# Kernel tuning notes

Hardware: AMD Instinct MI355X
Metric: run time of the kernel (lower is better)

Reference implementation:

```python
import jax, jax.numpy as jnp
import numpy as np

B, M, D, H, W = 8, 36, 512, 14, 14
T = 64
HW = H * W
N = M * HW
GAMMA1, GAMMA2, GAMMA3 = 4.0, 5.0, 10.0


def setup_inputs() -> dict:
    key = jax.random.key(0)
    k1, k2 = jax.random.split(key)
    image = jax.random.normal(k1, (B, M, D, H, W), dtype=jnp.float32) * 0.1
    text = jax.random.normal(k2, (B, T, D), dtype=jnp.float32) * 0.1
    length_info = jnp.full((B,), T, dtype=jnp.int32)
    rng = np.random.RandomState(0)
    sp = rng.randint(0, B, size=(B, 5)).astype(np.int32)
    sp[:, 0] = np.arange(B)  # spinds[0] = i in the original loop
    spinds = jnp.asarray(sp)
    return {"image": image, "text": text, "length_info": length_info, "spinds": spinds}


def matching_score(v, e):
    """v: (N, D) flattened region features, e: (T, D) word features.
    Returns (scalar score R_QD + R_QD2, beta (T, M))."""
    sim = e @ v.T                                   # (T, N)
    norm_sim = jax.nn.softmax(sim, axis=0)          # softmax over words
    attn = jax.nn.softmax(GAMMA1 * norm_sim, axis=1)  # softmax over regions
    v_tidal = attn @ v                              # (T, D)
    diag = jnp.sum(v_tidal * e, axis=1)             # diag(v_tidal @ e.T), (T,)
    r_qd = (1.0 / GAMMA2) * jnp.log(jnp.sum(jnp.exp(diag * GAMMA2)))

    sim_exp = jnp.exp(norm_sim).reshape(T, M, HW)
    local_sum = jnp.sum(sim_exp, axis=(0, 2))       # (M,) per-box total
    beta = jnp.sum(sim_exp, axis=2) / local_sum     # (T, M)

    e_prime = e.T @ beta                            # (D, M)
    v_r = v.reshape(M, HW, D)
    ve = jnp.einsum('mnd,dm->mn', v_r, e_prime)     # (M, HW)
    row_norm = jnp.linalg.norm(v_r, axis=2)         # (M, HW)
    ep_norm = jnp.linalg.norm(e_prime, axis=0)      # (M,)
    ref = jnp.sum(ve / (row_norm * ep_norm[:, None]), axis=1) / HW  # (M,)
    r_qd2 = (1.0 / GAMMA2) * jnp.log(jnp.sum(jnp.exp(ref)))
    return r_qd + r_qd2, beta


def _forward(image, text, spinds):
    # permute(0,3,2,1) then view(M*H_r*H_w, D): (M, D, H, W) -> (M, W, H, D)
    v_all = jnp.transpose(image, (0, 1, 4, 3, 2)).reshape(B, N, D)

    # pairwise matching score S[i, j] = score(v_i, e_j)
    S = jax.vmap(lambda vi: jax.vmap(lambda ej: matching_score(vi, ej)[0])(text))(v_all)  # (B, B)
    betas = jax.vmap(lambda vi, ei: matching_score(vi, ei)[1])(v_all, text)               # (B, T, M)

    numer = GAMMA3 * jnp.exp(jnp.diagonal(S))                       # (B,)
    # P_DQ_denum_i = sum_k gamma3 * exp(S[i, spinds[i,k]])
    p_dq = jnp.sum(GAMMA3 * jnp.exp(jnp.take_along_axis(S, spinds, axis=1)), axis=1)
    # P_QD_denum_i = sum_k gamma3 * exp(S[spinds[i,k], i])
    p_qd = jnp.sum(GAMMA3 * jnp.exp(jnp.take_along_axis(S.T, spinds, axis=1)), axis=1)

    loss1 = -jnp.mean(numer / p_dq)
    loss2 = -jnp.mean(numer / p_qd)

    tmp = jnp.einsum('btm,bsm->bts', betas, betas)                  # (B, T, T)
    diag2 = jnp.sum(jnp.diagonal(tmp, axis1=1, axis2=2) ** 2, axis=1)
    reg = jnp.sum(jnp.sqrt(jnp.sum(tmp ** 2, axis=(1, 2)) - diag2))
    loss_reg = reg / (B * T * M)
    return loss1 + loss2 + loss_reg


def reference(image, text, length_info, spinds):
    # length_info is full (== T) for every sample, so each e = text[i][:T].
    return _forward(image, text, spinds)
```

## Files before the change

kernel.cpp:

```cpp
#include <hip/hip_runtime.h>
#include <hip/hip_bf16.h>
#include <cstdint>

#define BB 8
#define MM 36
#define DD 512
#define TT 64
#define HWW 196
#define HWP 224
#define NN 7056
#define NNP 8064
#define NCK 252
#define NPAIR 64
#define G2c 5.0f
#define G3c 10.0f

typedef __attribute__((ext_vector_type(8))) short s8v;
typedef __attribute__((ext_vector_type(4))) float f4v;

__device__ __forceinline__ float bflySum(float v) {
#pragma unroll
  for (int off = 32; off > 0; off >>= 1) v += __shfl_xor(v, off, 64);
  return v;
}
__device__ __forceinline__ float bflyMax(float v) {
#pragma unroll
  for (int off = 32; off > 0; off >>= 1) v = fmaxf(v, __shfl_xor(v, off, 64));
  return v;
}
__device__ __forceinline__ unsigned short f2bf(float x) {
  __hip_bfloat16 h = __float2bfloat16(x);
  return *(unsigned short*)&h;
}
__device__ __forceinline__ float bf2f(unsigned short u) {
  unsigned int x = ((unsigned int)u) << 16;
  return __uint_as_float(x);
}

__global__ void p_text(const float* __restrict__ text,
                       unsigned short* __restrict__ eb) {
  int idx = blockIdx.x * 256 + threadIdx.x;
  eb[idx] = f2bf(text[idx]);
}

__global__ void __launch_bounds__(256) p_img(const float* __restrict__ image,
                                             unsigned int* __restrict__ imgbp) {
  int bm = blockIdx.x, ds = blockIdx.y;
  int tid = threadIdx.x;
  const float* src = image + ((size_t)bm * DD + ds * 32) * HWW;
  unsigned int* dst = imgbp + ((size_t)bm * DD + ds * 32) * (HWP / 2);
#pragma unroll
  for (int u = 0; u < 14; ++u) {
    int idx = tid + u * 256;
    int dl = idx / 112, hp = idx - dl * 112;
    int hw = hp * 2;
    unsigned int lo = 0, hi = 0;
    if (hp < 98) {
      lo = f2bf(src[(size_t)dl * HWW + hw]);
      hi = f2bf(src[(size_t)dl * HWW + hw + 1]);
    }
    dst[(size_t)dl * (HWP / 2) + hp] = lo | (hi << 16);
  }
}

__global__ void p_imgT(const float* __restrict__ image,
                       unsigned short* __restrict__ imgbp2) {
  __shared__ float tile[32][33];
  int bm = blockIdx.x;
  int hw0 = blockIdx.y * 32;
  int d0 = blockIdx.z * 32;
  int tx = threadIdx.x, ty = threadIdx.y;
  const float* src = image + ((size_t)bm * DD + d0) * HWW + hw0;
#pragma unroll
  for (int r = 0; r < 32; r += 8) {
    int d = r + ty;
    tile[d][tx] = (hw0 + tx < HWW) ? src[(size_t)d * HWW + tx] : 0.f;
  }
  __syncthreads();
  unsigned short* dst = imgbp2 + ((size_t)bm * HWP + hw0) * DD + d0;
#pragma unroll
  for (int r = 0; r < 32; r += 8) {
    int hwo = r + ty;
    dst[(size_t)hwo * DD + tx] = f2bf(tile[tx][hwo]);
  }
}

__global__ void __launch_bounds__(256) k1_mfma(
    const unsigned short* __restrict__ eb,
    const unsigned short* __restrict__ imgbp2,
    unsigned short* __restrict__ attnR,
    float* __restrict__ wpartg, float* __restrict__ apartg) {
  int ck = blockIdx.x;
  int i = blockIdx.y;
  int mi = ck / 7;
  int hwb = (ck - mi * 7) * 32;
  int bm = i * MM + mi;
  int tid = threadIdx.x;
  int w = tid >> 6, l = tid & 63;
  int g = l >> 4, c = l & 15;

  __shared__ unsigned short vsb[32][520];
  __shared__ unsigned short trb[512 * 32];

  const unsigned short* vsrc = imgbp2 + ((size_t)bm * HWP + hwb) * DD;
#pragma unroll
  for (int k = 0; k < 8; ++k) {
    int flat = tid * 8 + k * 2048;
    int row = flat >> 9, col = flat & 511;
    *(s8v*)&vsb[row][col] = *(const s8v*)(vsrc + (size_t)row * DD + col);
  }
  __syncthreads();

  f4v acc[8][2];
#pragma unroll
  for (int q = 0; q < 8; ++q)
#pragma unroll
    for (int nt = 0; nt < 2; ++nt) acc[q][nt] = (f4v){0.f, 0.f, 0.f, 0.f};

  for (int ks = 0; ks < 16; ++ks) {
    int d0 = ks * 32;
    s8v Bf0 = *(const s8v*)&vsb[c][d0 + g * 8];
    s8v Bf1 = *(const s8v*)&vsb[16 + c][d0 + g * 8];
#pragma unroll
    for (int q = 0; q < 8; ++q) {
      s8v Af = *(const s8v*)(eb + ((size_t)((w * 8 + q) * 16 + c)) * DD + d0 +
                             g * 8);
      acc[q][0] = __builtin_amdgcn_mfma_f32_16x16x32_bf16(Af, Bf0, acc[q][0], 0, 0, 0);
      acc[q][1] = __builtin_amdgcn_mfma_f32_16x16x32_bf16(Af, Bf1, acc[q][1], 0, 0, 0);
    }
  }

  float rz[2][2];
#pragma unroll
  for (int jj = 0; jj < 2; ++jj)
#pragma unroll
    for (int nt = 0; nt < 2; ++nt) {
      float mx = -3e38f;
#pragma unroll
      for (int qq = 0; qq < 4; ++qq)
#pragma unroll
        for (int r = 0; r < 4; ++r) mx = fmaxf(mx, acc[jj * 4 + qq][nt][r]);
      mx = fmaxf(mx, __shfl_xor(mx, 16, 64));
      mx = fmaxf(mx, __shfl_xor(mx, 32, 64));
      float z = 0.f;
#pragma unroll
      for (int qq = 0; qq < 4; ++qq)
#pragma unroll
        for (int r = 0; r < 4; ++r) {
          float p = expf(acc[jj * 4 + qq][nt][r] - mx);
          acc[jj * 4 + qq][nt][r] = p;
          z += p;
        }
      z += __shfl_xor(z, 16, 64);
      z += __shfl_xor(z, 32, 64);
      rz[jj][nt] = 1.f / z;
    }

#pragma unroll
  for (int q = 0; q < 8; ++q) {
    int jj = q >> 2;
#pragma unroll
    for (int r = 0; r < 4; ++r) {
      float wp = 0.f, ap = 0.f;
#pragma unroll
      for (int nt = 0; nt < 2; ++nt) {
        float ns = acc[q][nt][r] * rz[jj][nt];
        float w1 = expf(ns);
        float a2 = w1 * w1;
        float a4 = a2 * a2;
        bool valid = (hwb + nt * 16 + c) < HWW;
        float a4m = valid ? a4 : 0.f;
        trb[((w * 8 + q) * 16 + g * 4 + r) * 32 + nt * 16 + c] = f2bf(a4m);
        wp += valid ? w1 : 0.f;
        ap += a4m;
      }
#pragma unroll
      for (int off = 1; off < 16; off <<= 1) {
        wp += __shfl_xor(wp, off, 64);
        ap += __shfl_xor(ap, off, 64);
      }
      if (c == 0) {
        int t = (q & 3) * 16 + g * 4 + r;
        size_t pidx = ((size_t)(i * 8 + 2 * w + jj) * NCK + ck) * 64 + t;
        wpartg[pidx] = wp;
        apartg[pidx] = ap;
      }
    }
  }
  __syncthreads();
#pragma unroll
  for (int j = 0; j < 8; ++j) {
    unsigned short* dst =
        attnR + ((size_t)(i * 8 + j) * NCK + ck) * 2048 + tid * 8;
    *(s8v*)dst = *(const s8v*)&trb[j * 2048 + tid * 8];
  }
}

__global__ void __launch_bounds__(256) k_red(const float* __restrict__ wpartg,
                                             const float* __restrict__ apartg,
                                             float* __restrict__ sbuf,
                                             float* __restrict__ Abuf) {
  int pair = blockIdx.x;
  int tid = threadIdx.x;
  int t = tid & 63, part = tid >> 6;
  float s = 0.f;
  for (int ck = part; ck < NCK; ck += 4)
    s += apartg[((size_t)pair * NCK + ck) * 64 + t];
  __shared__ float ab[4][64];
  ab[part][t] = s;
  __syncthreads();
  if (tid < 64)
    Abuf[pair * 64 + tid] = ab[0][tid] + ab[1][tid] + ab[2][tid] + ab[3][tid];
  for (int idx = tid; idx < 64 * MM; idx += 256) {
    int tt = idx / MM, m = idx - (idx / MM) * MM;
    float ss = 0.f;
#pragma unroll
    for (int cc = 0; cc < 7; ++cc)
      ss += wpartg[((size_t)pair * NCK + m * 7 + cc) * 64 + tt];
    sbuf[((size_t)pair * TT + tt) * MM + m] = ss;
  }
}

__global__ void __launch_bounds__(256) k2_mfma(
    const unsigned short* __restrict__ attnR,
    const unsigned short* __restrict__ imgbp, float* __restrict__ vt_part) {
  int dh = blockIdx.x;
  int kslab = blockIdx.y;
  int pair = blockIdx.z;
  int i = pair >> 3;
  int tid = threadIdx.x;
  int w = tid >> 6, l = tid & 63;
  int g = l >> 4, c = l & 15;
  int d0b = dh * 256;

  __shared__ unsigned short asb[TT][40];
  __shared__ unsigned short bsb[256][40];

  f4v acc[4][4];
#pragma unroll
  for (int tt = 0; tt < 4; ++tt)
#pragma unroll
    for (int dd = 0; dd < 4; ++dd) acc[tt][dd] = (f4v){0.f, 0.f, 0.f, 0.f};

  for (int ks = 0; ks < 126; ++ks) {
    int ckg = kslab * 126 + ks;
    int n0 = ckg * 32;
    int mi = n0 / HWP, hw0 = n0 - mi * HWP;
    const unsigned short* bbase =
        imgbp + ((size_t)(i * MM + mi) * DD + d0b) * HWP + hw0;
    __syncthreads();
    {
      const unsigned short* ach = attnR + ((size_t)pair * NCK + ckg) * 2048;
      int t = tid >> 2, qq = tid & 3;
      *(s8v*)&asb[t][qq * 8] = *(const s8v*)(ach + tid * 8);
    }
#pragma unroll
    for (int u = 0; u < 4; ++u) {
      int idx = tid + u * 256;
      int d = idx >> 2, qq = idx & 3;
      *(s8v*)&bsb[d][qq * 8] = *(const s8v*)(bbase + (size_t)d * HWP + qq * 8);
    }
    __syncthreads();
    s8v Af[4];
#pragma unroll
    for (int tt = 0; tt < 4; ++tt)
      Af[tt] = *(const s8v*)&asb[tt * 16 + c][g * 8];
#pragma unroll
    for (int dd = 0; dd < 4; ++dd) {
      s8v Bf = *(const s8v*)&bsb[(w * 4 + dd) * 16 + c][g * 8];
#pragma unroll
      for (int tt = 0; tt < 4; ++tt)
        acc[tt][dd] = __builtin_amdgcn_mfma_f32_16x16x32_bf16(Af[tt], Bf,
                                                              acc[tt][dd], 0, 0, 0);
    }
  }
  float* op = vt_part + ((size_t)kslab * NPAIR + pair) * TT * DD;
#pragma unroll
  for (int tt = 0; tt < 4; ++tt)
#pragma unroll
    for (int dd = 0; dd < 4; ++dd)
#pragma unroll
      for (int r = 0; r < 4; ++r) {
        int t = tt * 16 + g * 4 + r;
        int d = d0b + (w * 4 + dd) * 16 + c;
        op[(size_t)t * DD + d] = acc[tt][dd][r];
      }
}

__global__ void __launch_bounds__(256) k2b_reduce(
    const float* __restrict__ vt_part, const float* __restrict__ Abuf,
    float* __restrict__ v_tidal) {
  size_t f = (size_t)blockIdx.x * 256 + threadIdx.x;
  size_t base = f * 4;
  const size_t slab = (size_t)NPAIR * TT * DD;
  float rA = 1.f / Abuf[base >> 9];
  float4 s0 = *(const float4*)&vt_part[base];
  float4 s1 = *(const float4*)&vt_part[slab + base];
  float4 r;
  r.x = (s0.x + s1.x) * rA;
  r.y = (s0.y + s1.y) * rA;
  r.z = (s0.z + s1.z) * rA;
  r.w = (s0.w + s1.w) * rA;
  *(float4*)&v_tidal[base] = r;
}

__global__ void __launch_bounds__(256) k3_rqd(
    const float* __restrict__ v_tidal, const float* __restrict__ text,
    float* __restrict__ r_qd) {
  int pair = blockIdx.x;
  int j = pair & 7;
  int lane = threadIdx.x & 63, wid = threadIdx.x >> 6;
  __shared__ float dg[TT];
  for (int tt = 0; tt < 16; ++tt) {
    int t = wid * 16 + tt;
    const float* vt = v_tidal + ((size_t)pair * TT + t) * DD;
    const float* e = text + ((size_t)j * TT + t) * DD;
    float a = 0.f;
#pragma unroll
    for (int k = 0; k < 8; ++k) {
      int d = k * 64 + lane;
      a = fmaf(vt[d], e[d], a);
    }
    a = bflySum(a);
    if (lane == 0) dg[t] = a;
  }
  __syncthreads();
  if (threadIdx.x < TT) {
    float v = dg[threadIdx.x] * G2c;
    float mxv = bflyMax(v);
    float zz = bflySum(expf(v - mxv));
    if (threadIdx.x == 0) r_qd[pair] = (mxv + logf(zz)) / G2c;
  }
}

__global__ void __launch_bounds__(256) k4_beta(const float* __restrict__ sbuf,
                                               float* __restrict__ beta) {
  int pair = blockIdx.x;
  __shared__ float sl[TT * MM];
  __shared__ float ls[MM];
  for (int idx = threadIdx.x; idx < TT * MM; idx += 256)
    sl[idx] = sbuf[(size_t)pair * TT * MM + idx];
  __syncthreads();
  if (threadIdx.x < MM) {
    float a = 0.f;
    for (int t = 0; t < TT; ++t) a += sl[t * MM + threadIdx.x];
    ls[threadIdx.x] = 1.f / a;
  }
  __syncthreads();
  for (int idx = threadIdx.x; idx < TT * MM; idx += 256) {
    int mcol = idx % MM;
    beta[(size_t)pair * TT * MM + idx] = sl[idx] * ls[mcol];
  }
}

__global__ void __launch_bounds__(256) k5_eprime(
    const float* __restrict__ text, const float* __restrict__ beta,
    float* __restrict__ e_prime, float* __restrict__ ep_norm) {
  int m = blockIdx.x, pair = blockIdx.y;
  int j = pair & 7;
  int d = threadIdx.x * 2;
  float a0 = 0.f, a1 = 0.f;
  const float* bt = beta + (size_t)pair * TT * MM + m;
  const float* e = text + (size_t)j * TT * DD + d;
  for (int t = 0; t < TT; ++t) {
    float b = bt[t * MM];
    float2 ev = *(const float2*)(e + (size_t)t * DD);
    a0 = fmaf(ev.x, b, a0);
    a1 = fmaf(ev.y, b, a1);
  }
  *(float2*)(e_prime + ((size_t)pair * MM + m) * DD + d) = make_float2(a0, a1);
  __shared__ float buf[4];
  float nr = bflySum(a0 * a0 + a1 * a1);
  int lane = threadIdx.x & 63, wid = threadIdx.x >> 6;
  if (lane == 0) buf[wid] = nr;
  __syncthreads();
  if (threadIdx.x == 0)
    ep_norm[pair * MM + m] = sqrtf(buf[0] + buf[1] + buf[2] + buf[3]);
}

__global__ void __launch_bounds__(256) k6_ref(
    const unsigned short* __restrict__ imgbp2,
    const float* __restrict__ e_prime, const float* __restrict__ ep_norm,
    float* __restrict__ refb) {
  int m = blockIdx.x, pair = blockIdx.y;
  int i = pair >> 3;
  int bm = i * MM + m;
  int tid = threadIdx.x, w = tid >> 6, l = tid & 63;
  const float* ep = e_prime + ((size_t)pair * MM + m) * DD + l * 8;
  float4 e0 = *(const float4*)ep;
  float4 e1 = *(const float4*)(ep + 4);
  float epr[8] = {e0.x, e0.y, e0.z, e0.w, e1.x, e1.y, e1.z, e1.w};
  float ren = 1.f / ep_norm[pair * MM + m];
  float accv = 0.f;
  for (int k = 0; k < 49; ++k) {
    int hw = w + 4 * k;
    s8v v8 = *(const s8v*)(imgbp2 + ((size_t)bm * HWP + hw) * DD + l * 8);
    float ve = 0.f, rn = 0.f;
#pragma unroll
    for (int e = 0; e < 8; ++e) {
      float vv = bf2f((unsigned short)v8[e]);
      ve = fmaf(vv, epr[e], ve);
      rn = fmaf(vv, vv, rn);
    }
    ve = bflySum(ve);
    rn = bflySum(rn);
    accv += ve * rsqrtf(rn) * ren;
  }
  __shared__ float buf[4];
  if (l == 0) buf[w] = accv;
  __syncthreads();
  if (tid == 0)
    refb[pair * MM + m] = (buf[0] + buf[1] + buf[2] + buf[3]) * (1.0f / HWW);
}

__global__ void k7_S(const float* __restrict__ refb,
                     const float* __restrict__ r_qd, float* __restrict__ Sb) {
  int pair = threadIdx.x;
  if (pair >= NPAIR) return;
  const float* r = refb + pair * MM;
  float mx = -1e30f;
  for (int mi = 0; mi < MM; ++mi) mx = fmaxf(mx, r[mi]);
  float z = 0.f;
  for (int mi = 0; mi < MM; ++mi) z += expf(r[mi] - mx);
  Sb[pair] = r_qd[pair] + (mx + logf(z)) / G2c;
}

__global__ void __launch_bounds__(256) k8a(const float* __restrict__ beta,
                                           float* __restrict__ sregs) {
  int b = blockIdx.x;
  __shared__ float bb[TT * MM];
  __shared__ float buf[4];
  int tid = threadIdx.x;
  size_t base = (size_t)(b * BB + b) * TT * MM;
  for (int idx = tid; idx < TT * MM; idx += 256) bb[idx] = beta[base + idx];
  __syncthreads();
  float val = 0.f;
  for (int k = 0; k < 16; ++k) {
    int idx = tid + k * 256;
    int t = idx >> 6, s2 = idx & 63;
    if (t != s2) {
      float dot = 0.f;
      for (int mi = 0; mi < MM; ++mi)
        dot = fmaf(bb[t * MM + mi], bb[s2 * MM + mi], dot);
      val += dot * dot;
    }
  }
  val = bflySum(val);
  int lane = tid & 63, wid = tid >> 6;
  if (lane == 0) buf[wid] = val;
  __syncthreads();
  if (tid == 0) sregs[b] = sqrtf(fmaxf(buf[0] + buf[1] + buf[2] + buf[3], 0.f));
}

__global__ void k8b(const float* __restrict__ Sb,
                    const float* __restrict__ sregs,
                    const int* __restrict__ spinds, float* __restrict__ out) {
  if (threadIdx.x != 0) return;
  float sreg = 0.f;
  for (int b = 0; b < BB; ++b) sreg += sregs[b];
  float l1 = 0.f, l2 = 0.f;
  for (int i = 0; i < BB; ++i) {
    float num = G3c * expf(Sb[i * BB + i]);
    float pdq = 0.f, pqd = 0.f;
    for (int k = 0; k < 5; ++k) {
      int kk = spinds[i * 5 + k];
      pdq += G3c * expf(Sb[i * BB + kk]);
      pqd += G3c * expf(Sb[kk * BB + i]);
    }
    l1 += num / pdq;
    l2 += num / pqd;
  }
  out[0] = -(l1 / BB) - (l2 / BB) + sreg / (float)(BB * TT * MM);
}

extern "C" void kernel_launch(void* const* d_in, const int* in_sizes, int n_in,
                              void* d_out, int out_size, void* d_ws,
                              size_t ws_size, hipStream_t stream) {
  const float* image = (const float*)d_in[0];
  const float* text = (const float*)d_in[1];
  const int* spinds = (const int*)d_in[3];
  float* out = (float*)d_out;

  float* ws = (float*)d_ws;
  size_t off = 0;
  unsigned short* attnR = (unsigned short*)(ws + off);
  off += (size_t)NPAIR * NCK * 2048 / 2;
  unsigned short* imgbp = (unsigned short*)(ws + off);
  off += (size_t)BB * MM * DD * HWP / 2;
  unsigned short* imgbp2 = (unsigned short*)(ws + off);
  off += (size_t)BB * MM * HWP * DD / 2;
  float* vt_part = ws + off; off += (size_t)2 * NPAIR * TT * DD;
  unsigned short* eb = (unsigned short*)(ws + off);
  off += (size_t)BB * TT * DD / 2;
  float* wpartg = ws + off;  off += (size_t)NPAIR * NCK * 64;
  float* apartg = ws + off;  off += (size_t)NPAIR * NCK * 64;
  float* Abuf = ws + off;    off += (size_t)NPAIR * TT;
  float* v_tidal = ws + off; off += (size_t)NPAIR * TT * DD;
  float* sbuf = ws + off;    off += (size_t)NPAIR * TT * MM;
  float* beta = ws + off;    off += (size_t)NPAIR * TT * MM;
  float* e_prime = ws + off; off += (size_t)NPAIR * MM * DD;
  float* ep_norm = ws + off; off += (size_t)NPAIR * MM;
  float* refb = ws + off;    off += (size_t)NPAIR * MM;
  float* r_qd = ws + off;    off += (size_t)NPAIR;
  float* Sb = ws + off;      off += (size_t)NPAIR;
  float* sregs = ws + off;   off += (size_t)BB;

  p_text<<<1024, 256, 0, stream>>>(text, eb);
  p_img<<<dim3(BB * MM, 16), 256, 0, stream>>>(image, (unsigned int*)imgbp);
  p_imgT<<<dim3(BB * MM, 7, 16), dim3(32, 8), 0, stream>>>(image, imgbp2);
  k1_mfma<<<dim3(NCK, BB), 256, 0, stream>>>(eb, imgbp2, attnR, wpartg, apartg);
  k_red<<<NPAIR, 256, 0, stream>>>(wpartg, apartg, sbuf, Abuf);
  k2_mfma<<<dim3(2, 2, NPAIR), 256, 0, stream>>>(attnR, imgbp, vt_part);
  k2b_reduce<<<2048, 256, 0, stream>>>(vt_part, Abuf, v_tidal);
  k3_rqd<<<NPAIR, 256, 0, stream>>>(v_tidal, text, r_qd);
  k4_beta<<<NPAIR, 256, 0, stream>>>(sbuf, beta);
  k5_eprime<<<dim3(MM, NPAIR), 256, 0, stream>>>(text, beta, e_prime, ep_norm);
  k6_ref<<<dim3(MM, NPAIR), 256, 0, stream>>>(imgbp2, e_prime, ep_norm, refb);
  k7_S<<<1, 64, 0, stream>>>(refb, r_qd, Sb);
  k8a<<<BB, 256, 0, stream>>>(beta, sregs);
  k8b<<<1, 64, 0, stream>>>(Sb, sregs, spinds, out);
}
```

Measured before the change: 718.3 us.

## Fuse preprocessing and small reduction kernels, swizzle k1 LDS, share image reads in k6

Merges the two image conversion kernels into one transpose pass that writes both bf16 layouts. It folds the beta normalisation into the partial-sum reduction, the v_tidal reduce into k3, and the S computation into the final loss kernel. In k1 it reuses one XOR-swizzled shared buffer for both the V tile and the transpose staging, which cuts LDS use and avoids bank conflicts. k6 now processes all 8 text pairs per image block, so each image row is read once rather than eight times. The goal is fewer launches and less global traffic, at the cost of more registers in k6 and an extra barrier in k1.

Result: faster. 658.7 us (-8.3%).

```diff
diff --git a/kernel.cpp b/kernel.cpp
--- a/kernel.cpp
+++ b/kernel.cpp
@@ -43,27 +43,8 @@
   eb[idx] = f2bf(text[idx]);
 }
 
-__global__ void __launch_bounds__(256) p_img(const float* __restrict__ image,
-                                             unsigned int* __restrict__ imgbp) {
-  int bm = blockIdx.x, ds = blockIdx.y;
-  int tid = threadIdx.x;
-  const float* src = image + ((size_t)bm * DD + ds * 32) * HWW;
-  unsigned int* dst = imgbp + ((size_t)bm * DD + ds * 32) * (HWP / 2);
-#pragma unroll
-  for (int u = 0; u < 14; ++u) {
-    int idx = tid + u * 256;
-    int dl = idx / 112, hp = idx - dl * 112;
-    int hw = hp * 2;
-    unsigned int lo = 0, hi = 0;
-    if (hp < 98) {
-      lo = f2bf(src[(size_t)dl * HWW + hw]);
-      hi = f2bf(src[(size_t)dl * HWW + hw + 1]);
-    }
-    dst[(size_t)dl * (HWP / 2) + hp] = lo | (hi << 16);
-  }
-}
-
-__global__ void p_imgT(const float* __restrict__ image,
+__global__ void p_img2(const float* __restrict__ image,
+                       unsigned short* __restrict__ imgbp,
                        unsigned short* __restrict__ imgbp2) {
   __shared__ float tile[32][33];
   int bm = blockIdx.x;
@@ -74,7 +55,9 @@
 #pragma unroll
   for (int r = 0; r < 32; r += 8) {
     int d = r + ty;
-    tile[d][tx] = (hw0 + tx < HWW) ? src[(size_t)d * HWW + tx] : 0.f;
+    float v = (hw0 + tx < HWW) ? src[(size_t)d * HWW + tx] : 0.f;
+    tile[d][tx] = v;
+    imgbp[((size_t)bm * DD + d0 + d) * HWP + hw0 + tx] = f2bf(v);
   }
   __syncthreads();
   unsigned short* dst = imgbp2 + ((size_t)bm * HWP + hw0) * DD + d0;
@@ -99,15 +82,15 @@
   int w = tid >> 6, l = tid & 63;
   int g = l >> 4, c = l & 15;
 
-  __shared__ unsigned short vsb[32][520];
-  __shared__ unsigned short trb[512 * 32];
+  __shared__ unsigned short smem[16384];
 
   const unsigned short* vsrc = imgbp2 + ((size_t)bm * HWP + hwb) * DD;
 #pragma unroll
   for (int k = 0; k < 8; ++k) {
-    int flat = tid * 8 + k * 2048;
-    int row = flat >> 9, col = flat & 511;
-    *(s8v*)&vsb[row][col] = *(const s8v*)(vsrc + (size_t)row * DD + col);
+    int r = (tid >> 6) + k * 4;
+    int u = tid & 63;
+    *(s8v*)&smem[r * 512 + ((u ^ (r & 7)) << 3)] =
+        *(const s8v*)(vsrc + (size_t)r * DD + (u << 3));
   }
   __syncthreads();
 
@@ -119,8 +102,9 @@
 
   for (int ks = 0; ks < 16; ++ks) {
     int d0 = ks * 32;
-    s8v Bf0 = *(const s8v*)&vsb[c][d0 + g * 8];
-    s8v Bf1 = *(const s8v*)&vsb[16 + c][d0 + g * 8];
+    int u = 4 * ks + g;
+    s8v Bf0 = *(const s8v*)&smem[c * 512 + ((u ^ (c & 7)) << 3)];
+    s8v Bf1 = *(const s8v*)&smem[(16 + c) * 512 + ((u ^ ((16 + c) & 7)) << 3)];
 #pragma unroll
     for (int q = 0; q < 8; ++q) {
       s8v Af = *(const s8v*)(eb + ((size_t)((w * 8 + q) * 16 + c)) * DD + d0 +
@@ -156,6 +140,8 @@
       rz[jj][nt] = 1.f / z;
     }
 
+  __syncthreads();
+
 #pragma unroll
   for (int q = 0; q < 8; ++q) {
     int jj = q >> 2;
@@ -170,7 +156,7 @@
         float a4 = a2 * a2;
         bool valid = (hwb + nt * 16 + c) < HWW;
         float a4m = valid ? a4 : 0.f;
-        trb[((w * 8 + q) * 16 + g * 4 + r) * 32 + nt * 16 + c] = f2bf(a4m);
+        smem[((w * 8 + q) * 16 + g * 4 + r) * 32 + nt * 16 + c] = f2bf(a4m);
         wp += valid ? w1 : 0.f;
         ap += a4m;
       }
@@ -192,14 +178,13 @@
   for (int j = 0; j < 8; ++j) {
     unsigned short* dst =
         attnR + ((size_t)(i * 8 + j) * NCK + ck) * 2048 + tid * 8;
-    *(s8v*)dst = *(const s8v*)&trb[j * 2048 + tid * 8];
-  }
-}
-
-__global__ void __launch_bounds__(256) k_red(const float* __restrict__ wpartg,
-                                             const float* __restrict__ apartg,
-                                             float* __restrict__ sbuf,
-                                             float* __restrict__ Abuf) {
+    *(s8v*)dst = *(const s8v*)&smem[j * 2048 + tid * 8];
+  }
+}
+
+__global__ void __launch_bounds__(256) k_redbeta(
+    const float* __restrict__ wpartg, const float* __restrict__ apartg,
+    float* __restrict__ beta, float* __restrict__ Abuf) {
   int pair = blockIdx.x;
   int tid = threadIdx.x;
   int t = tid & 63, part = tid >> 6;
@@ -211,14 +196,25 @@
   __syncthreads();
   if (tid < 64)
     Abuf[pair * 64 + tid] = ab[0][tid] + ab[1][tid] + ab[2][tid] + ab[3][tid];
-  for (int idx = tid; idx < 64 * MM; idx += 256) {
+  __shared__ float sl[TT * MM];
+  for (int idx = tid; idx < TT * MM; idx += 256) {
     int tt = idx / MM, m = idx - (idx / MM) * MM;
     float ss = 0.f;
 #pragma unroll
     for (int cc = 0; cc < 7; ++cc)
       ss += wpartg[((size_t)pair * NCK + m * 7 + cc) * 64 + tt];
-    sbuf[((size_t)pair * TT + tt) * MM + m] = ss;
-  }
+    sl[idx] = ss;
+  }
+  __syncthreads();
+  __shared__ float ls[MM];
+  if (tid < MM) {
+    float a = 0.f;
+    for (int tq = 0; tq < TT; ++tq) a += sl[tq * MM + tid];
+    ls[tid] = 1.f / a;
+  }
+  __syncthreads();
+  for (int idx = tid; idx < TT * MM; idx += 256)
+    beta[(size_t)pair * TT * MM + idx] = sl[idx] * ls[idx % MM];
 }
 
 __global__ void __launch_bounds__(256) k2_mfma(
@@ -287,42 +283,26 @@
       }
 }
 
-__global__ void __launch_bounds__(256) k2b_reduce(
+__global__ void __launch_bounds__(256) k3_rqd(
     const float* __restrict__ vt_part, const float* __restrict__ Abuf,
-    float* __restrict__ v_tidal) {
-  size_t f = (size_t)blockIdx.x * 256 + threadIdx.x;
-  size_t base = f * 4;
-  const size_t slab = (size_t)NPAIR * TT * DD;
-  float rA = 1.f / Abuf[base >> 9];
-  float4 s0 = *(const float4*)&vt_part[base];
-  float4 s1 = *(const float4*)&vt_part[slab + base];
-  float4 r;
-  r.x = (s0.x + s1.x) * rA;
-  r.y = (s0.y + s1.y) * rA;
-  r.z = (s0.z + s1.z) * rA;
-  r.w = (s0.w + s1.w) * rA;
-  *(float4*)&v_tidal[base] = r;
-}
-
-__global__ void __launch_bounds__(256) k3_rqd(
-    const float* __restrict__ v_tidal, const float* __restrict__ text,
-    float* __restrict__ r_qd) {
+    const float* __restrict__ text, float* __restrict__ r_qd) {
   int pair = blockIdx.x;
   int j = pair & 7;
+  const size_t slab = (size_t)NPAIR * TT * DD;
   int lane = threadIdx.x & 63, wid = threadIdx.x >> 6;
   __shared__ float dg[TT];
   for (int tt = 0; tt < 16; ++tt) {
     int t = wid * 16 + tt;
-    const float* vt = v_tidal + ((size_t)pair * TT + t) * DD;
+    const float* vt = vt_part + ((size_t)pair * TT + t) * DD;
     const float* e = text + ((size_t)j * TT + t) * DD;
     float a = 0.f;
 #pragma unroll
     for (int k = 0; k < 8; ++k) {
       int d = k * 64 + lane;
-      a = fmaf(vt[d], e[d], a);
+      a = fmaf(vt[d] + vt[slab + d], e[d], a);
     }
     a = bflySum(a);
-    if (lane == 0) dg[t] = a;
+    if (lane == 0) dg[t] = a / Abuf[pair * 64 + t];
   }
   __syncthreads();
   if (threadIdx.x < TT) {
@@ -330,26 +310,6 @@
     float mxv = bflyMax(v);
     float zz = bflySum(expf(v - mxv));
     if (threadIdx.x == 0) r_qd[pair] = (mxv + logf(zz)) / G2c;
-  }
-}
-
-__global__ void __launch_bounds__(256) k4_beta(const float* __restrict__ sbuf,
-                                               float* __restrict__ beta) {
-  int pair = blockIdx.x;
-  __shared__ float sl[TT * MM];
-  __shared__ float ls[MM];
-  for (int idx = threadIdx.x; idx < TT * MM; idx += 256)
-    sl[idx] = sbuf[(size_t)pair * TT * MM + idx];
-  __syncthreads();
-  if (threadIdx.x < MM) {
-    float a = 0.f;
-    for (int t = 0; t < TT; ++t) a += sl[t * MM + threadIdx.x];
-    ls[threadIdx.x] = 1.f / a;
-  }
-  __syncthreads();
-  for (int idx = threadIdx.x; idx < TT * MM; idx += 256) {
-    int mcol = idx % MM;
-    beta[(size_t)pair * TT * MM + idx] = sl[idx] * ls[mcol];
   }
 }
 
@@ -382,47 +342,55 @@
     const unsigned short* __restrict__ imgbp2,
     const float* __restrict__ e_prime, const float* __restrict__ ep_norm,
     float* __restrict__ refb) {
-  int m = blockIdx.x, pair = blockIdx.y;
-  int i = pair >> 3;
+  int m = blockIdx.x, i = blockIdx.y;
   int bm = i * MM + m;
   int tid = threadIdx.x, w = tid >> 6, l = tid & 63;
-  const float* ep = e_prime + ((size_t)pair * MM + m) * DD + l * 8;
-  float4 e0 = *(const float4*)ep;
-  float4 e1 = *(const float4*)(ep + 4);
-  float epr[8] = {e0.x, e0.y, e0.z, e0.w, e1.x, e1.y, e1.z, e1.w};
-  float ren = 1.f / ep_norm[pair * MM + m];
-  float accv = 0.f;
+  float epr[8][8];
+  float ren[8];
+#pragma unroll
+  for (int j = 0; j < 8; ++j) {
+    int pair = i * 8 + j;
+    const float* ep = e_prime + ((size_t)pair * MM + m) * DD + l * 8;
+    float4 e0 = *(const float4*)ep;
+    float4 e1 = *(const float4*)(ep + 4);
+    epr[j][0] = e0.x; epr[j][1] = e0.y; epr[j][2] = e0.z; epr[j][3] = e0.w;
+    epr[j][4] = e1.x; epr[j][5] = e1.y; epr[j][6] = e1.z; epr[j][7] = e1.w;
+    ren[j] = 1.f / ep_norm[pair * MM + m];
+  }
+  float accv[8];
+#pragma unroll
+  for (int j = 0; j < 8; ++j) accv[j] = 0.f;
   for (int k = 0; k < 49; ++k) {
     int hw = w + 4 * k;
     s8v v8 = *(const s8v*)(imgbp2 + ((size_t)bm * HWP + hw) * DD + l * 8);
-    float ve = 0.f, rn = 0.f;
+    float vv[8];
+    float rn = 0.f;
 #pragma unroll
     for (int e = 0; e < 8; ++e) {
-      float vv = bf2f((unsigned short)v8[e]);
-      ve = fmaf(vv, epr[e], ve);
-      rn = fmaf(vv, vv, rn);
-    }
-    ve = bflySum(ve);
+      vv[e] = bf2f((unsigned short)v8[e]);
+      rn = fmaf(vv[e], vv[e], rn);
+    }
     rn = bflySum(rn);
-    accv += ve * rsqrtf(rn) * ren;
-  }
-  __shared__ float buf[4];
-  if (l == 0) buf[w] = accv;
-  __syncthreads();
-  if (tid == 0)
-    refb[pair * MM + m] = (buf[0] + buf[1] + buf[2] + buf[3]) * (1.0f / HWW);
-}
-
-__global__ void k7_S(const float* __restrict__ refb,
-                     const float* __restrict__ r_qd, float* __restrict__ Sb) {
-  int pair = threadIdx.x;
-  if (pair >= NPAIR) return;
-  const float* r = refb + pair * MM;
-  float mx = -1e30f;
-  for (int mi = 0; mi < MM; ++mi) mx = fmaxf(mx, r[mi]);
-  float z = 0.f;
-  for (int mi = 0; mi < MM; ++mi) z += expf(r[mi] - mx);
-  Sb[pair] = r_qd[pair] + (mx + logf(z)) / G2c;
+    float rs = rsqrtf(rn);
+#pragma unroll
+    for (int j = 0; j < 8; ++j) {
+      float ve = 0.f;
+#pragma unroll
+      for (int e = 0; e < 8; ++e) ve = fmaf(vv[e], epr[j][e], ve);
+      ve = bflySum(ve);
+      accv[j] += ve * rs * ren[j];
+    }
+  }
+  __shared__ float buf[4][8];
+  if (l == 0) {
+#pragma unroll
+    for (int j = 0; j < 8; ++j) buf[w][j] = accv[j];
+  }
+  __syncthreads();
+  if (tid < 8) {
+    float s = buf[0][tid] + buf[1][tid] + buf[2][tid] + buf[3][tid];
+    refb[(i * 8 + tid) * MM + m] = s * (1.0f / HWW);
+  }
 }
 
 __global__ void __launch_bounds__(256) k8a(const float* __restrict__ beta,
@@ -452,25 +420,39 @@
   if (tid == 0) sregs[b] = sqrtf(fmaxf(buf[0] + buf[1] + buf[2] + buf[3], 0.f));
 }
 
-__global__ void k8b(const float* __restrict__ Sb,
-                    const float* __restrict__ sregs,
-                    const int* __restrict__ spinds, float* __restrict__ out) {
-  if (threadIdx.x != 0) return;
-  float sreg = 0.f;
-  for (int b = 0; b < BB; ++b) sreg += sregs[b];
-  float l1 = 0.f, l2 = 0.f;
-  for (int i = 0; i < BB; ++i) {
-    float num = G3c * expf(Sb[i * BB + i]);
-    float pdq = 0.f, pqd = 0.f;
-    for (int k = 0; k < 5; ++k) {
-      int kk = spinds[i * 5 + k];
-      pdq += G3c * expf(Sb[i * BB + kk]);
-      pqd += G3c * expf(Sb[kk * BB + i]);
-    }
-    l1 += num / pdq;
-    l2 += num / pqd;
-  }
-  out[0] = -(l1 / BB) - (l2 / BB) + sreg / (float)(BB * TT * MM);
+__global__ void k8_final(const float* __restrict__ refb,
+                         const float* __restrict__ r_qd,
+                         const float* __restrict__ sregs,
+                         const int* __restrict__ spinds,
+                         float* __restrict__ out) {
+  __shared__ float Sl[NPAIR];
+  int tid = threadIdx.x;
+  if (tid < NPAIR) {
+    const float* r = refb + tid * MM;
+    float mx = -1e30f;
+    for (int mi = 0; mi < MM; ++mi) mx = fmaxf(mx, r[mi]);
+    float z = 0.f;
+    for (int mi = 0; mi < MM; ++mi) z += expf(r[mi] - mx);
+    Sl[tid] = r_qd[tid] + (mx + logf(z)) / G2c;
+  }
+  __syncthreads();
+  if (tid == 0) {
+    float sreg = 0.f;
+    for (int b = 0; b < BB; ++b) sreg += sregs[b];
+    float l1 = 0.f, l2 = 0.f;
+    for (int i = 0; i < BB; ++i) {
+      float num = G3c * expf(Sl[i * BB + i]);
+      float pdq = 0.f, pqd = 0.f;
+      for (int k = 0; k < 5; ++k) {
+        int kk = spinds[i * 5 + k];
+        pdq += G3c * expf(Sl[i * BB + kk]);
+        pqd += G3c * expf(Sl[kk * BB + i]);
+      }
+      l1 += num / pdq;
+      l2 += num / pqd;
+    }
+    out[0] = -(l1 / BB) - (l2 / BB) + sreg / (float)(BB * TT * MM);
+  }
 }
 
 extern "C" void kernel_launch(void* const* d_in, const int* in_sizes, int n_in,
@@ -495,28 +477,22 @@
   float* wpartg = ws + off;  off += (size_t)NPAIR * NCK * 64;
   float* apartg = ws + off;  off += (size_t)NPAIR * NCK * 64;
   float* Abuf = ws + off;    off += (size_t)NPAIR * TT;
-  float* v_tidal = ws + off; off += (size_t)NPAIR * TT * DD;
-  float* sbuf = ws + off;    off += (size_t)NPAIR * TT * MM;
   float* beta = ws + off;    off += (size_t)NPAIR * TT * MM;
   float* e_prime = ws + off; off += (size_t)NPAIR * MM * DD;
   float* ep_norm = ws + off; off += (size_t)NPAIR * MM;
   float* refb = ws + off;    off += (size_t)NPAIR * MM;
   float* r_qd = ws + off;    off += (size_t)NPAIR;
-  float* Sb = ws + off;      off += (size_t)NPAIR;
   float* sregs = ws + off;   off += (size_t)BB;
 
   p_text<<<1024, 256, 0, stream>>>(text, eb);
-  p_img<<<dim3(BB * MM, 16), 256, 0, stream>>>(image, (unsigned int*)imgbp);
-  p_imgT<<<dim3(BB * MM, 7, 16), dim3(32, 8), 0, stream>>>(image, imgbp2);
+  p_img2<<<dim3(BB * MM, 7, 16), dim3(32, 8), 0, stream>>>(image, imgbp,
+                                                           imgbp2);
   k1_mfma<<<dim3(NCK, BB), 256, 0, stream>>>(eb, imgbp2, attnR, wpartg, apartg);
-  k_red<<<NPAIR, 256, 0, stream>>>(wpartg, apartg, sbuf, Abuf);
+  k_redbeta<<<NPAIR, 256, 0, stream>>>(wpartg, apartg, beta, Abuf);
   k2_mfma<<<dim3(2, 2, NPAIR), 256, 0, stream>>>(attnR, imgbp, vt_part);
-  k2b_reduce<<<2048, 256, 0, stream>>>(vt_part, Abuf, v_tidal);
-  k3_rqd<<<NPAIR, 256, 0, stream>>>(v_tidal, text, r_qd);
-  k4_beta<<<NPAIR, 256, 0, stream>>>(sbuf, beta);
+  k3_rqd<<<NPAIR, 256, 0, stream>>>(vt_part, Abuf, text, r_qd);
   k5_eprime<<<dim3(MM, NPAIR), 256, 0, stream>>>(text, beta, e_prime, ep_norm);
-  k6_ref<<<dim3(MM, NPAIR), 256, 0, stream>>>(imgbp2, e_prime, ep_norm, refb);
-  k7_S<<<1, 64, 0, stream>>>(refb, r_qd, Sb);
+  k6_ref<<<dim3(MM, BB), 256, 0, stream>>>(imgbp2, e_prime, ep_norm, refb);
   k8a<<<BB, 256, 0, stream>>>(beta, sregs);
-  k8b<<<1, 64, 0, stream>>>(Sb, sregs, spinds, out);
-}
+  k8_final<<<1, 64, 0, stream>>>(refb, r_qd, sregs, spinds, out);
+}
```
